# Kernel tuning notes

Measured on AMD Instinct MI355X. Metric: run time of the kernel, lower is better.

## Reference

```python
import jax, jax.numpy as jnp
import numpy as np
import math

B, S, D = 8, 1024, 1024
NH, NKV, HD = 16, 8, 64
BLK_NUM, BLK_SIZE = 128, 8

def apply_rope(x, cos, sin):
    # x: (B,S,H,HD); cos/sin: (S, HD//2)
    x1 = x[..., 0::2]
    x2 = x[..., 1::2]
    c = cos[None, :, None, :]
    s = sin[None, :, None, :]
    r1 = x1 * c - x2 * s
    r2 = x1 * s + x2 * c
    out = jnp.stack([r1, r2], axis=-1).reshape(x.shape)
    return out

def setup_inputs() -> dict:
    key = jax.random.key(0)
    ks = jax.random.split(key, 7)
    x = jax.random.normal(ks[0], (B, S, D), dtype=jnp.float32)
    scale = 1.0 / math.sqrt(D)
    wq = jax.random.normal(ks[1], (D, NH * HD), dtype=jnp.float32) * scale
    wk = jax.random.normal(ks[2], (D, NKV * HD), dtype=jnp.float32) * scale
    wv = jax.random.normal(ks[3], (D, NKV * HD), dtype=jnp.float32) * scale
    wo = jax.random.normal(ks[4], (NH * HD, D), dtype=jnp.float32) * scale
    pos = jnp.arange(S, dtype=jnp.float32)
    inv_freq = 1.0 / (10000.0 ** (jnp.arange(0, HD, 2, dtype=jnp.float32) / HD))
    ang = pos[:, None] * inv_freq[None, :]
    freqs_cis_cos = jnp.cos(ang)
    freqs_cis_sin = jnp.sin(ang)
    return {"x": x, "wq": wq, "wk": wk, "wv": wv, "wo": wo,
            "freqs_cis_cos": freqs_cis_cos, "freqs_cis_sin": freqs_cis_sin,
            "start_pos": 0}

def reference(x, wq, wk, wv, wo, freqs_cis_cos, freqs_cis_sin, start_pos):
    q = (x @ wq).reshape(B, S, NH, HD)
    k = (x @ wk).reshape(B, S, NKV, HD)
    v = (x @ wv).reshape(B, S, NKV, HD)
    q = apply_rope(q, freqs_cis_cos, freqs_cis_sin)
    k = apply_rope(k, freqs_cis_cos, freqs_cis_sin)
    # GQA: repeat kv heads
    rep = NH // NKV
    k = jnp.repeat(k, rep, axis=2)  # (B,S,NH,HD)
    v = jnp.repeat(v, rep, axis=2)
    # block-causal mask: q in block i attends to kv blocks j <= i
    blk_id = jnp.arange(S) // BLK_SIZE
    mask = blk_id[:, None] >= blk_id[None, :]  # (S,S)
    scores = jnp.einsum('bqhd,bkhd->bhqk', q, k) / math.sqrt(HD)
    scores = jnp.where(mask[None, None], scores, -jnp.inf)
    attn = jax.nn.softmax(scores, axis=-1)
    out = jnp.einsum('bhqk,bkhd->bqhd', attn, v).reshape(B, S, NH * HD)
    return out @ wo
```

## Files before the change

### kernel.cpp

```cpp
#include <hip/hip_runtime.h>
#include <cstdint>
#include <math.h>

#define B_   8
#define S_   1024
#define D_   1024
#define NH_  16
#define NKV_ 8
#define HD_  64
#define M_   (B_*S_)

using bf16   = __bf16;
using bf16x4 = __attribute__((ext_vector_type(4))) __bf16;
using bf16x8 = __attribute__((ext_vector_type(8))) __bf16;
using f32x4  = __attribute__((ext_vector_type(4))) float;

__device__ __forceinline__ void gll16(const bf16* g, const bf16* l) {
    __builtin_amdgcn_global_load_lds(
        (const __attribute__((address_space(1))) unsigned int*)(uintptr_t)g,
        (__attribute__((address_space(3))) unsigned int*)(uintptr_t)l,
        16, 0, 0);
}

__global__ void k_cvt_bf16(const float* __restrict__ in, bf16* __restrict__ out, int n4) {
    int i = blockIdx.x * blockDim.x + threadIdx.x;
    if (i < n4) {
        float4 v = ((const float4*)in)[i];
        bf16x4 o = { (bf16)v.x, (bf16)v.y, (bf16)v.z, (bf16)v.w };
        ((bf16x4*)out)[i] = o;
    }
}

__global__ void k_transpose_all(const float* __restrict__ wq, const float* __restrict__ wk,
                                const float* __restrict__ wv, const float* __restrict__ wo,
                                bf16* __restrict__ wqkvT, bf16* __restrict__ woT) {
    __shared__ float tile[64 * 65];
    const int R = 1024;
    int bx = blockIdx.x;
    const float* in; bf16* out; int C, xo;
    if (bx < 16)      { in = wq; out = wqkvT;               C = 1024; xo = bx; }
    else if (bx < 24) { in = wk; out = wqkvT + 1024 * 1024; C = 512;  xo = bx - 16; }
    else if (bx < 32) { in = wv; out = wqkvT + 1536 * 1024; C = 512;  xo = bx - 24; }
    else              { in = wo; out = woT;                 C = 1024; xo = bx - 32; }
    int r0 = blockIdx.y * 64, c0 = xo * 64;
    int t = threadIdx.x;
    #pragma unroll
    for (int it = 0; it < 16; ++it) {
        int idx = it * 256 + t;
        int r = idx >> 6, c = idx & 63;
        tile[r * 65 + c] = in[(size_t)(r0 + r) * C + c0 + c];
    }
    __syncthreads();
    #pragma unroll
    for (int it = 0; it < 16; ++it) {
        int idx = it * 256 + t;
        int c = idx >> 6, r = idx & 63;
        out[(size_t)(c0 + c) * R + r0 + r] = (bf16)tile[r * 65 + c];
    }
}

template <typename OutT>
__global__ __launch_bounds__(256) void k_gemm_bt(const bf16* __restrict__ A, const bf16* __restrict__ Bt,
                                                 OutT* __restrict__ C, int M, int N, int K) {
    __shared__ __align__(16) bf16 aLds[128 * 64];
    __shared__ __align__(16) bf16 bLds[128 * 64];
    const int t    = threadIdx.x;
    const int lane = t & 63;
    const int w    = t >> 6;
    const int quad = lane >> 4;
    const int l16  = lane & 15;
    const int m0 = blockIdx.y * 128;
    const int n0 = blockIdx.x * 128;
    const int rm = (w >> 1) * 64;
    const int rn = (w & 1) * 64;

    f32x4 acc[4][4] = {};

    const int nkb = K >> 6;
    for (int kb = 0; kb < nkb; ++kb) {
        const int k0 = kb << 6;
        __syncthreads();
        #pragma unroll
        for (int it = 0; it < 4; ++it) {
            int ci = it * 256 + t;
            int r = ci >> 3, c = ci & 7;
            int cg = c ^ (r & 7);
            gll16(A  + (size_t)(m0 + r) * K + k0 + cg * 8, aLds + ci * 8);
            gll16(Bt + (size_t)(n0 + r) * K + k0 + cg * 8, bLds + ci * 8);
        }
        __syncthreads();
        #pragma unroll
        for (int kk = 0; kk < 2; ++kk) {
            bf16x8 af[4], bf[4];
            #pragma unroll
            for (int mi = 0; mi < 4; ++mi) {
                int row = rm + mi * 16 + l16;
                int ch  = (kk * 4 + quad) ^ (row & 7);
                af[mi] = *(const bf16x8*)&aLds[row * 64 + ch * 8];
            }
            #pragma unroll
            for (int ni = 0; ni < 4; ++ni) {
                int row = rn + ni * 16 + l16;
                int ch  = (kk * 4 + quad) ^ (row & 7);
                bf[ni] = *(const bf16x8*)&bLds[row * 64 + ch * 8];
            }
            #pragma unroll
            for (int mi = 0; mi < 4; ++mi)
                #pragma unroll
                for (int ni = 0; ni < 4; ++ni)
                    acc[mi][ni] = __builtin_amdgcn_mfma_f32_16x16x32_bf16(af[mi], bf[ni], acc[mi][ni], 0, 0, 0);
        }
    }
    #pragma unroll
    for (int mi = 0; mi < 4; ++mi)
        #pragma unroll
        for (int ni = 0; ni < 4; ++ni)
            #pragma unroll
            for (int r = 0; r < 4; ++r) {
                int row = m0 + rm + mi * 16 + quad * 4 + r;
                int col = n0 + rn + ni * 16 + l16;
                C[(size_t)row * N + col] = (OutT)acc[mi][ni][r];
            }
}

__global__ void k_rope(const bf16* __restrict__ qkv, const float* __restrict__ cosg,
                       const float* __restrict__ sing, bf16* __restrict__ qd, bf16* __restrict__ kd) {
    int token = blockIdx.x;
    int b = token >> 10, s = token & 1023;
    int t = threadIdx.x;
    #pragma unroll
    for (int it = 0; it < 3; ++it) {
        int u = it * 256 + t;
        int hh = u >> 5, i = u & 31;
        float c = cosg[s * 32 + i], sn = sing[s * 32 + i];
        int srcBase, dstBase;
        bf16* dst;
        float sf;
        if (hh < 16) {
            srcBase = token * 2048 + hh * 64;
            dstBase = ((b * NH_ + hh) * S_ + s) * 64;
            dst = qd;
            sf = 0.180336879f;
        } else {
            int h = hh - 16;
            srcBase = token * 2048 + 1024 + h * 64;
            dstBase = ((b * NKV_ + h) * S_ + s) * 64;
            dst = kd;
            sf = 1.0f;
        }
        float e = (float)qkv[srcBase + 2 * i];
        float o = (float)qkv[srcBase + 2 * i + 1];
        dst[dstBase + 2 * i]     = (bf16)(sf * (e * c - o * sn));
        dst[dstBase + 2 * i + 1] = (bf16)(sf * (e * sn + o * c));
    }
}

__global__ void k_vtrans(const bf16* __restrict__ qkv, bf16* __restrict__ vt) {
    __shared__ __align__(16) bf16 tile[64 * 72];
    int bid = blockIdx.x;
    int st = bid & 15;
    int h  = (bid >> 4) & 7;
    int b  = bid >> 7;
    int s0 = st * 64;
    int t = threadIdx.x;
    #pragma unroll
    for (int it = 0; it < 2; ++it) {
        int ci = it * 256 + t;
        int r = ci >> 3, c = ci & 7;
        *(uint4*)&tile[r * 72 + c * 8] =
            *(const uint4*)&qkv[(size_t)(b * S_ + s0 + r) * 2048 + 1536 + h * 64 + c * 8];
    }
    __syncthreads();
    #pragma unroll
    for (int it = 0; it < 2; ++it) {
        int ci = it * 256 + t;
        int d = ci >> 3, sc = ci & 7;
        int g = sc >> 2, q4 = sc & 3;
        bf16x8 v;
        #pragma unroll
        for (int j = 0; j < 8; ++j) {
            int s_ext = g * 32 + q4 * 4 + (j & 3) + 16 * (j >> 2);
            v[j] = tile[s_ext * 72 + d];
        }
        *(bf16x8*)&vt[(size_t)((b * NKV_ + h) * 64 + d) * S_ + s0 + sc * 8] = v;
    }
}

__global__ __launch_bounds__(256) void k_attn(const bf16* __restrict__ q, const bf16* __restrict__ k,
                                              const bf16* __restrict__ vt, bf16* __restrict__ out) {
    __shared__ __align__(16) bf16 kt[64 * 64];
    __shared__ __align__(16) bf16 vtt[64 * 64];
    int bid = blockIdx.x;
    int pi = bid & 7;
    int h  = (bid >> 3) & 15;
    int b  = bid >> 7;
    int qtA = pi, qtB = 15 - pi;
    int hkv = h >> 1;
    int t = threadIdx.x;
    int w = t >> 6, lane = t & 63, quad = lane >> 4, l16 = lane & 15;

    const bf16* qh = q + (size_t)(b * NH_ + h) * S_ * 64;
    int qwA = qtA * 64 + w * 16, qwB = qtB * 64 + w * 16;
    const bf16* qbA = qh + (size_t)(qwA + l16) * 64;
    const bf16* qbB = qh + (size_t)(qwB + l16) * 64;
    bf16x8 qfA0 = *(const bf16x8*)(qbA + quad * 8);
    bf16x8 qfA1 = *(const bf16x8*)(qbA + 32 + quad * 8);
    bf16x8 qfB0 = *(const bf16x8*)(qbB + quad * 8);
    bf16x8 qfB1 = *(const bf16x8*)(qbB + 32 + quad * 8);

    const bf16* kg = k  + (size_t)(b * NKV_ + hkv) * S_ * 64;
    const bf16* vg = vt + (size_t)(b * NKV_ + hkv) * 64 * S_;

    const int sr0 = t >> 3;
    const int cs  = t & 7;

    auto stage = [&](int k0) {
        #pragma unroll
        for (int it = 0; it < 2; ++it) {
            int r  = sr0 + it * 32;
            int cg = cs ^ (r & 7);
            int ci = it * 256 + t;
            gll16(kg + (size_t)(k0 + r) * 64 + cg * 8, kt  + ci * 8);
            gll16(vg + (size_t)r * S_ + k0 + cg * 8,   vtt + ci * 8);
        }
    };

    const bf16 one = (bf16)1.0f;
    const bf16x8 vones = { one, one, one, one, one, one, one, one };

    f32x4 o[4] = {};
    f32x4 ol = {};
    bf16x8 qf0 = qfA0, qf1 = qfA1;
    int qw = qwA;

    auto epilogue = [&]() {
        #pragma unroll
        for (int r = 0; r < 4; ++r) {
            float invl = 1.0f / ol[r];
            #pragma unroll
            for (int dc = 0; dc < 4; ++dc) {
                int row = qw + quad * 4 + r;
                int col = h * 64 + dc * 16 + l16;
                out[(size_t)(b * S_ + row) * 1024 + col] = (bf16)(o[dc][r] * invl);
            }
        }
    };

    const int NU = 17;
    for (int u = 0; u < NU; ++u) {
        int kti = (u > qtA) ? (u - qtA - 1) : u;
        int k0  = kti * 64;
        __syncthreads();
        stage(k0);
        __syncthreads();

        f32x4 sc[4] = {};
        #pragma unroll
        for (int kk = 0; kk < 2; ++kk)
            #pragma unroll
            for (int f = 0; f < 4; ++f) {
                int row = f * 16 + l16;
                int ch  = (kk * 4 + quad) ^ (row & 7);
                bf16x8 af = *(const bf16x8*)&kt[row * 64 + ch * 8];
                sc[f] = __builtin_amdgcn_mfma_f32_16x16x32_bf16(af, kk ? qf1 : qf0, sc[f], 0, 0, 0);
            }

        bool diag = (u == qtA) || (u == NU - 1);
        int klim = ((qw + l16) & ~7) + 8;
        float p[4][4];
        #pragma unroll
        for (int f = 0; f < 4; ++f)
            #pragma unroll
            for (int r = 0; r < 4; ++r) {
                float pv = exp2f(sc[f][r]);
                if (diag && (k0 + f * 16 + quad * 4 + r >= klim)) pv = 0.f;
                p[f][r] = pv;
            }

        bf16x8 pa0, pa1;
        #pragma unroll
        for (int j = 0; j < 4; ++j) {
            pa0[j]     = (bf16)p[0][j];
            pa0[j + 4] = (bf16)p[1][j];
            pa1[j]     = (bf16)p[2][j];
            pa1[j + 4] = (bf16)p[3][j];
        }

        ol = __builtin_amdgcn_mfma_f32_16x16x32_bf16(pa0, vones, ol, 0, 0, 0);
        ol = __builtin_amdgcn_mfma_f32_16x16x32_bf16(pa1, vones, ol, 0, 0, 0);

        #pragma unroll
        for (int dc = 0; dc < 4; ++dc) {
            int row = dc * 16 + l16;
            #pragma unroll
            for (int kk = 0; kk < 2; ++kk) {
                int ch = (kk * 4 + quad) ^ (row & 7);
                bf16x8 vb = *(const bf16x8*)&vtt[row * 64 + ch * 8];
                o[dc] = __builtin_amdgcn_mfma_f32_16x16x32_bf16(kk ? pa1 : pa0, vb, o[dc], 0, 0, 0);
            }
        }

        if (u == qtA) {
            epilogue();
            #pragma unroll
            for (int dc = 0; dc < 4; ++dc) o[dc] = f32x4{0.f, 0.f, 0.f, 0.f};
            ol = f32x4{0.f, 0.f, 0.f, 0.f};
            qf0 = qfB0; qf1 = qfB1; qw = qwB;
        }
    }
    epilogue();
}

extern "C" void kernel_launch(void* const* d_in, const int* in_sizes, int n_in,
                              void* d_out, int out_size, void* d_ws, size_t ws_size,
                              hipStream_t stream) {
    const float* x  = (const float*)d_in[0];
    const float* wq = (const float*)d_in[1];
    const float* wk = (const float*)d_in[2];
    const float* wv = (const float*)d_in[3];
    const float* wo = (const float*)d_in[4];
    const float* fc = (const float*)d_in[5];
    const float* fs = (const float*)d_in[6];
    (void)in_sizes; (void)n_in; (void)out_size; (void)ws_size;

    char* ws = (char*)d_ws;
    bf16* xb    = (bf16*)(ws);
    bf16* wqkvT = (bf16*)(ws + (16u << 20));
    bf16* woT   = (bf16*)(ws + (20u << 20));
    bf16* qkvb  = (bf16*)(ws + (22u << 20));
    bf16* kb    = (bf16*)(ws + (54u << 20));
    bf16* vtb   = (bf16*)(ws + (62u << 20));
    bf16* qb    = xb;
    bf16* attnb = qkvb;

    k_cvt_bf16<<<dim3(8192), dim3(256), 0, stream>>>(x, xb, (M_ * D_) / 4);
    k_transpose_all<<<dim3(48, 16), dim3(256), 0, stream>>>(wq, wk, wv, wo, wqkvT, woT);

    k_gemm_bt<bf16><<<dim3(16, 64), dim3(256), 0, stream>>>(xb, wqkvT, qkvb, M_, 2048, 1024);

    k_rope<<<dim3(8192), dim3(256), 0, stream>>>(qkvb, fc, fs, qb, kb);
    k_vtrans<<<dim3(1024), dim3(256), 0, stream>>>(qkvb, vtb);

    k_attn<<<dim3(1024), dim3(256), 0, stream>>>(qb, kb, vtb, attnb);

    k_gemm_bt<float><<<dim3(8, 64), dim3(256), 0, stream>>>(attnb, woT, (float*)d_out, M_, 1024, 1024);
}
```

Baseline: 230.8 us.

## Double-buffer GEMM and attention LDS staging, enlarge GEMM tiles, vectorize RoPE

Replaces the 128x128 GEMM with a 256xBN tile kernel that uses 512 threads and double-buffered LDS, so the next K-slice loads while MFMAs run. The attention kernel likewise double-buffers its K/V tiles and uses a single barrier per iteration. RoPE now processes 8 elements per thread with vector loads and stores. The larger tiles raise register and LDS pressure, which may reduce occupancy, and the QKV GEMM grid shrinks to 256 blocks.

```diff
diff --git a/kernel.cpp b/kernel.cpp
--- a/kernel.cpp
+++ b/kernel.cpp
@@ -21,6 +21,9 @@
         (__attribute__((address_space(3))) unsigned int*)(uintptr_t)l,
         16, 0, 0);
 }
+
+__device__ __forceinline__ void vm_wait0()  { asm volatile("s_waitcnt vmcnt(0)" ::: "memory"); }
+__device__ __forceinline__ void bar()       { __builtin_amdgcn_s_barrier(); asm volatile("" ::: "memory"); }
 
 __global__ void k_cvt_bf16(const float* __restrict__ in, bf16* __restrict__ out, int n4) {
     int i = blockIdx.x * blockDim.x + threadIdx.x;
@@ -59,66 +62,88 @@
     }
 }
 
-template <typename OutT>
-__global__ __launch_bounds__(256) void k_gemm_bt(const bf16* __restrict__ A, const bf16* __restrict__ Bt,
-                                                 OutT* __restrict__ C, int M, int N, int K) {
-    __shared__ __align__(16) bf16 aLds[128 * 64];
-    __shared__ __align__(16) bf16 bLds[128 * 64];
+template <typename OutT, int BN>
+__global__ __launch_bounds__(512, 2) void k_gemm256(const bf16* __restrict__ A,
+                                                    const bf16* __restrict__ Bt,
+                                                    OutT* __restrict__ C, int M, int N, int K) {
+    constexpr int NI = BN / 64;
+    constexpr int NB = (BN * 8) / 512;
+    __shared__ __align__(16) bf16 aLds[2 * 256 * 64];
+    __shared__ __align__(16) bf16 bLds[2 * BN * 64];
     const int t    = threadIdx.x;
     const int lane = t & 63;
     const int w    = t >> 6;
     const int quad = lane >> 4;
     const int l16  = lane & 15;
-    const int m0 = blockIdx.y * 128;
-    const int n0 = blockIdx.x * 128;
-    const int rm = (w >> 1) * 64;
-    const int rn = (w & 1) * 64;
-
-    f32x4 acc[4][4] = {};
-
-    const int nkb = K >> 6;
-    for (int kb = 0; kb < nkb; ++kb) {
+    const int wr   = w >> 2;
+    const int wc   = w & 3;
+    const int m0 = blockIdx.y * 256;
+    const int n0 = blockIdx.x * BN;
+
+    f32x4 acc[8][NI] = {};
+
+    auto stage = [&](int kb, int buf) {
         const int k0 = kb << 6;
-        __syncthreads();
         #pragma unroll
         for (int it = 0; it < 4; ++it) {
-            int ci = it * 256 + t;
+            int ci = it * 512 + t;
             int r = ci >> 3, c = ci & 7;
             int cg = c ^ (r & 7);
-            gll16(A  + (size_t)(m0 + r) * K + k0 + cg * 8, aLds + ci * 8);
-            gll16(Bt + (size_t)(n0 + r) * K + k0 + cg * 8, bLds + ci * 8);
-        }
-        __syncthreads();
+            gll16(A + (size_t)(m0 + r) * K + k0 + cg * 8, aLds + buf * (256 * 64) + ci * 8);
+        }
+        #pragma unroll
+        for (int it = 0; it < NB; ++it) {
+            int ci = it * 512 + t;
+            int r = ci >> 3, c = ci & 7;
+            int cg = c ^ (r & 7);
+            gll16(Bt + (size_t)(n0 + r) * K + k0 + cg * 8, bLds + buf * (BN * 64) + ci * 8);
+        }
+    };
+
+    const int NT = K >> 6;
+    stage(0, 0);
+    vm_wait0();
+    bar();
+
+    for (int T = 0; T < NT; ++T) {
+        const int buf = T & 1;
+        if (T + 1 < NT) stage(T + 1, buf ^ 1);
+
+        const bf16* aL = aLds + buf * (256 * 64);
+        const bf16* bL = bLds + buf * (BN * 64);
         #pragma unroll
         for (int kk = 0; kk < 2; ++kk) {
-            bf16x8 af[4], bf[4];
-            #pragma unroll
-            for (int mi = 0; mi < 4; ++mi) {
-                int row = rm + mi * 16 + l16;
+            bf16x8 af[8], bfr[NI];
+            #pragma unroll
+            for (int mi = 0; mi < 8; ++mi) {
+                int row = wr * 128 + mi * 16 + l16;
                 int ch  = (kk * 4 + quad) ^ (row & 7);
-                af[mi] = *(const bf16x8*)&aLds[row * 64 + ch * 8];
-            }
-            #pragma unroll
-            for (int ni = 0; ni < 4; ++ni) {
-                int row = rn + ni * 16 + l16;
+                af[mi] = *(const bf16x8*)&aL[row * 64 + ch * 8];
+            }
+            #pragma unroll
+            for (int ni = 0; ni < NI; ++ni) {
+                int row = wc * (NI * 16) + ni * 16 + l16;
                 int ch  = (kk * 4 + quad) ^ (row & 7);
-                bf[ni] = *(const bf16x8*)&bLds[row * 64 + ch * 8];
-            }
-            #pragma unroll
-            for (int mi = 0; mi < 4; ++mi)
+                bfr[ni] = *(const bf16x8*)&bL[row * 64 + ch * 8];
+            }
+            #pragma unroll
+            for (int mi = 0; mi < 8; ++mi)
                 #pragma unroll
-                for (int ni = 0; ni < 4; ++ni)
-                    acc[mi][ni] = __builtin_amdgcn_mfma_f32_16x16x32_bf16(af[mi], bf[ni], acc[mi][ni], 0, 0, 0);
-        }
-    }
-    #pragma unroll
-    for (int mi = 0; mi < 4; ++mi)
-        #pragma unroll
-        for (int ni = 0; ni < 4; ++ni)
+                for (int ni = 0; ni < NI; ++ni)
+                    acc[mi][ni] = __builtin_amdgcn_mfma_f32_16x16x32_bf16(af[mi], bfr[ni], acc[mi][ni], 0, 0, 0);
+        }
+        vm_wait0();
+        bar();
+    }
+
+    #pragma unroll
+    for (int mi = 0; mi < 8; ++mi)
+        #pragma unroll
+        for (int ni = 0; ni < NI; ++ni)
             #pragma unroll
             for (int r = 0; r < 4; ++r) {
-                int row = m0 + rm + mi * 16 + quad * 4 + r;
-                int col = n0 + rn + ni * 16 + l16;
+                int row = m0 + wr * 128 + mi * 16 + quad * 4 + r;
+                int col = n0 + wc * (NI * 16) + ni * 16 + l16;
                 C[(size_t)row * N + col] = (OutT)acc[mi][ni][r];
             }
 }
@@ -128,31 +153,36 @@
     int token = blockIdx.x;
     int b = token >> 10, s = token & 1023;
     int t = threadIdx.x;
-    #pragma unroll
-    for (int it = 0; it < 3; ++it) {
-        int u = it * 256 + t;
-        int hh = u >> 5, i = u & 31;
-        float c = cosg[s * 32 + i], sn = sing[s * 32 + i];
-        int srcBase, dstBase;
-        bf16* dst;
-        float sf;
-        if (hh < 16) {
-            srcBase = token * 2048 + hh * 64;
-            dstBase = ((b * NH_ + hh) * S_ + s) * 64;
-            dst = qd;
-            sf = 0.180336879f;
-        } else {
-            int h = hh - 16;
-            srcBase = token * 2048 + 1024 + h * 64;
-            dstBase = ((b * NKV_ + h) * S_ + s) * 64;
-            dst = kd;
-            sf = 1.0f;
-        }
-        float e = (float)qkv[srcBase + 2 * i];
-        float o = (float)qkv[srcBase + 2 * i + 1];
-        dst[dstBase + 2 * i]     = (bf16)(sf * (e * c - o * sn));
-        dst[dstBase + 2 * i + 1] = (bf16)(sf * (e * sn + o * c));
-    }
+    int hh = t >> 3, i8 = t & 7;
+    float4 c4 = *(const float4*)&cosg[s * 32 + i8 * 4];
+    float4 s4 = *(const float4*)&sing[s * 32 + i8 * 4];
+    int srcBase, dstBase;
+    bf16* dst;
+    float sf;
+    if (hh < 16) {
+        srcBase = token * 2048 + hh * 64;
+        dstBase = ((b * NH_ + hh) * S_ + s) * 64;
+        dst = qd;
+        sf = 0.180336879f;
+    } else {
+        int h = hh - 16;
+        srcBase = token * 2048 + 1024 + h * 64;
+        dstBase = ((b * NKV_ + h) * S_ + s) * 64;
+        dst = kd;
+        sf = 1.0f;
+    }
+    bf16x8 v = *(const bf16x8*)&qkv[srcBase + i8 * 8];
+    const float cc[4] = { c4.x, c4.y, c4.z, c4.w };
+    const float ss[4] = { s4.x, s4.y, s4.z, s4.w };
+    bf16x8 o;
+    #pragma unroll
+    for (int j = 0; j < 4; ++j) {
+        float e  = (float)v[2 * j];
+        float od = (float)v[2 * j + 1];
+        o[2 * j]     = (bf16)(sf * (e * cc[j] - od * ss[j]));
+        o[2 * j + 1] = (bf16)(sf * (e * ss[j] + od * cc[j]));
+    }
+    *(bf16x8*)&dst[dstBase + i8 * 8] = o;
 }
 
 __global__ void k_vtrans(const bf16* __restrict__ qkv, bf16* __restrict__ vt) {
@@ -188,8 +218,8 @@
 
 __global__ __launch_bounds__(256) void k_attn(const bf16* __restrict__ q, const bf16* __restrict__ k,
                                               const bf16* __restrict__ vt, bf16* __restrict__ out) {
-    __shared__ __align__(16) bf16 kt[64 * 64];
-    __shared__ __align__(16) bf16 vtt[64 * 64];
+    __shared__ __align__(16) bf16 kt[2 * 64 * 64];
+    __shared__ __align__(16) bf16 vtt[2 * 64 * 64];
     int bid = blockIdx.x;
     int pi = bid & 7;
     int h  = (bid >> 3) & 15;
@@ -214,14 +244,14 @@
     const int sr0 = t >> 3;
     const int cs  = t & 7;
 
-    auto stage = [&](int k0) {
+    auto stage = [&](int k0, int buf) {
         #pragma unroll
         for (int it = 0; it < 2; ++it) {
             int r  = sr0 + it * 32;
             int cg = cs ^ (r & 7);
             int ci = it * 256 + t;
-            gll16(kg + (size_t)(k0 + r) * 64 + cg * 8, kt  + ci * 8);
-            gll16(vg + (size_t)r * S_ + k0 + cg * 8,   vtt + ci * 8);
+            gll16(kg + (size_t)(k0 + r) * 64 + cg * 8, kt  + buf * 4096 + ci * 8);
+            gll16(vg + (size_t)r * S_ + k0 + cg * 8,   vtt + buf * 4096 + ci * 8);
         }
     };
 
@@ -247,12 +277,21 @@
     };
 
     const int NU = 17;
+    stage(0, 0);
+    vm_wait0();
+    bar();
+
     for (int u = 0; u < NU; ++u) {
+        const int buf = u & 1;
+        if (u + 1 < NU) {
+            int un   = u + 1;
+            int ktiN = (un > qtA) ? (un - qtA - 1) : un;
+            stage(ktiN * 64, buf ^ 1);
+        }
         int kti = (u > qtA) ? (u - qtA - 1) : u;
         int k0  = kti * 64;
-        __syncthreads();
-        stage(k0);
-        __syncthreads();
+        const bf16* ktb = kt  + buf * 4096;
+        const bf16* vtb = vtt + buf * 4096;
 
         f32x4 sc[4] = {};
         #pragma unroll
@@ -261,7 +300,7 @@
             for (int f = 0; f < 4; ++f) {
                 int row = f * 16 + l16;
                 int ch  = (kk * 4 + quad) ^ (row & 7);
-                bf16x8 af = *(const bf16x8*)&kt[row * 64 + ch * 8];
+                bf16x8 af = *(const bf16x8*)&ktb[row * 64 + ch * 8];
                 sc[f] = __builtin_amdgcn_mfma_f32_16x16x32_bf16(af, kk ? qf1 : qf0, sc[f], 0, 0, 0);
             }
 
@@ -295,7 +334,7 @@
             #pragma unroll
             for (int kk = 0; kk < 2; ++kk) {
                 int ch = (kk * 4 + quad) ^ (row & 7);
-                bf16x8 vb = *(const bf16x8*)&vtt[row * 64 + ch * 8];
+                bf16x8 vb = *(const bf16x8*)&vtb[row * 64 + ch * 8];
                 o[dc] = __builtin_amdgcn_mfma_f32_16x16x32_bf16(kk ? pa1 : pa0, vb, o[dc], 0, 0, 0);
             }
         }
@@ -307,6 +346,9 @@
             ol = f32x4{0.f, 0.f, 0.f, 0.f};
             qf0 = qfB0; qf1 = qfB1; qw = qwB;
         }
+
+        vm_wait0();
+        bar();
     }
     epilogue();
 }
@@ -336,12 +378,12 @@
     k_cvt_bf16<<<dim3(8192), dim3(256), 0, stream>>>(x, xb, (M_ * D_) / 4);
     k_transpose_all<<<dim3(48, 16), dim3(256), 0, stream>>>(wq, wk, wv, wo, wqkvT, woT);
 
-    k_gemm_bt<bf16><<<dim3(16, 64), dim3(256), 0, stream>>>(xb, wqkvT, qkvb, M_, 2048, 1024);
-
-    k_rope<<<dim3(8192), dim3(256), 0, stream>>>(qkvb, fc, fs, qb, kb);
+    k_gemm256<bf16, 256><<<dim3(8, 32), dim3(512), 0, stream>>>(xb, wqkvT, qkvb, M_, 2048, 1024);
+
+    k_rope<<<dim3(8192), dim3(192), 0, stream>>>(qkvb, fc, fs, qb, kb);
     k_vtrans<<<dim3(1024), dim3(256), 0, stream>>>(qkvb, vtb);
 
     k_attn<<<dim3(1024), dim3(256), 0, stream>>>(qb, kb, vtb, attnb);
 
-    k_gemm_bt<float><<<dim3(8, 64), dim3(256), 0, stream>>>(attnb, woT, (float*)d_out, M_, 1024, 1024);
-}
+    k_gemm256<float, 128><<<dim3(8, 32), dim3(512), 0, stream>>>(attnb, woT, (float*)d_out, M_, 1024, 1024);
+}
```

After: 220.4 us. 1.05x faster.
